# Kernel optimization log

Measured on AMD Instinct MI355X. Metric: run time of the kernel, lower is better.

The kernel has to match this reference:

```python
import jax, jax.numpy as jnp
import numpy as np

K_SAMPLES = 1024   # number of farthest-point samples (self.K)
K_NEIGH = 64       # neighbors per ball (self.k_classes)
RADIUS = 0.2       # ball-query radius
LAYERS = [64, 64, 128]
IN_CH = 3


def _fps_indices(pts, k):
    """Iterative farthest point sampling (pytorch3d-style, start at index 0).
    pts: (B, N, D) -> idx: (B, k) int32."""
    B, N, D = pts.shape
    big = jnp.asarray(1e10, pts.dtype)

    def step(carry, _):
        min_d, last = carry                                   # (B,N), (B,)
        lp = jnp.take_along_axis(pts, last[:, None, None], axis=1)  # (B,1,D)
        d = jnp.sum((pts - lp) ** 2, axis=-1)                 # (B,N)
        min_d = jnp.minimum(min_d, d)
        nxt = jnp.argmax(min_d, axis=-1).astype(jnp.int32)    # farthest so far
        return (min_d, nxt), nxt

    init = (jnp.full((B, N), big, pts.dtype), jnp.zeros((B,), jnp.int32))
    _, rest = jax.lax.scan(step, init, None, length=k - 1)    # (k-1, B)
    idx = jnp.concatenate([jnp.zeros((1, B), jnp.int32), rest], axis=0)
    return idx.T                                              # (B, k)


def _ball_query(queries, pts, k, radius):
    """For each query take the first k points of pts within radius (by index
    order, as in pytorch3d.ball_query); pad missing neighbors with zeros.
    queries: (B,K,D), pts: (B,N,D) -> grouped: (B,K,k,D)."""
    B, N, D = pts.shape
    q2 = jnp.sum(queries ** 2, axis=-1)                       # (B,K)
    p2 = jnp.sum(pts ** 2, axis=-1)                           # (B,N)
    d2 = q2[:, :, None] + p2[:, None, :] - 2.0 * jnp.einsum('bkd,bnd->bkn', queries, pts)
    valid = d2 < radius * radius                              # (B,K,N)
    arange_n = jnp.arange(N, dtype=jnp.int32)
    key = jnp.where(valid, arange_n, N)                       # invalid -> sentinel N
    neg_vals, nbr_idx = jax.lax.top_k(-key, k)                # k smallest keys
    taken_valid = (-neg_vals) < N                             # (B,K,k)
    grouped = jax.vmap(lambda p, i: p[i])(pts, nbr_idx)       # (B,K,k,D)
    grouped = jnp.where(taken_valid[..., None], grouped, jnp.zeros((), pts.dtype))
    return grouped


def setup_inputs() -> dict:
    key = jax.random.key(0)
    ks = jax.random.split(key, 7)
    points = jax.random.uniform(ks[0], (8, 4096, IN_CH), dtype=jnp.float32)
    dims = [IN_CH] + LAYERS
    inp = {'points': points}
    for li in range(len(LAYERS)):
        fan_in = dims[li]
        w = jax.random.normal(ks[1 + li], (dims[li], dims[li + 1]), dtype=jnp.float32) / np.sqrt(fan_in)
        b = jnp.zeros((dims[li + 1],), jnp.float32)
        inp[f'w{li}'] = w
        inp[f'b{li}'] = b
    return inp


def reference(points, w0, b0, w1, b1, w2, b2):
    # 1) farthest point sampling of K centroids
    fps_idx = _fps_indices(points, K_SAMPLES)                 # (B,K)
    selected = jax.vmap(lambda p, i: p[i])(points, fps_idx)   # (B,K,C)
    selected_xyz = selected[:, :, :3]
    # 2) ball query grouping around the centroids
    grouped = _ball_query(selected, points, K_NEIGH, RADIUS)  # (B,K,k,C)
    # 3) shared PointNet MLP (pointwise 1x1 conv == linear) + max-pool over neighbors
    h = grouped
    for w, b in ((w0, b0), (w1, b1), (w2, b2)):
        h = jax.nn.relu(jnp.einsum('bknc,cd->bknd', h, w) + b)
    feat = jnp.max(h, axis=2)                                 # (B,K,layers[-1])
    # 4) concat centroid xyz with pooled features
    return jnp.concatenate([selected_xyz, feat], axis=2)      # (B,K,3+128)
```

## Files before the change

### kernel.cpp

```cpp
#include <hip/hip_runtime.h>

#define BATCH 8
#define NPTS 4096
#define KSAMP 1024
#define KNEI 64
#define OUTC 131

typedef __attribute__((ext_vector_type(8))) short  bf16x8;
typedef __attribute__((ext_vector_type(4))) float  f32x4;

__device__ __forceinline__ unsigned short f2bf_rne(float f)
{
    unsigned u = __float_as_uint(f);
    return (unsigned short)((u + 0x7FFFu + ((u >> 16) & 1u)) >> 16);
}
__device__ __forceinline__ float bf2f(unsigned short h)
{
    return __uint_as_float(((unsigned)h) << 16);
}

__device__ __forceinline__ unsigned long long umax64(unsigned long long a,
                                                     unsigned long long b)
{
    return a > b ? a : b;
}

#define DPP_U64_STEP(v, CTRL)                                                  \
    {                                                                          \
        int _lo = __builtin_amdgcn_update_dpp(0, (int)(unsigned)(v), (CTRL),   \
                                              0xF, 0xF, true);                 \
        int _hi = __builtin_amdgcn_update_dpp(0, (int)((v) >> 32), (CTRL),     \
                                              0xF, 0xF, true);                 \
        unsigned long long _o =                                                \
            ((unsigned long long)(unsigned)_hi << 32) | (unsigned)_lo;         \
        (v) = umax64((v), _o);                                                 \
    }

__device__ __forceinline__ unsigned long long wave_umax64(unsigned long long v)
{
    DPP_U64_STEP(v, 0x111)
    DPP_U64_STEP(v, 0x112)
    DPP_U64_STEP(v, 0x114)
    DPP_U64_STEP(v, 0x118)
    DPP_U64_STEP(v, 0x142)
    DPP_U64_STEP(v, 0x143)
    return v;
}

#define DPP_F32MAX_STEP(v, CTRL)                                               \
    {                                                                          \
        int _s = __builtin_amdgcn_update_dpp(0, __float_as_int(v), (CTRL),     \
                                             0xF, 0xF, true);                  \
        (v) = fmaxf((v), __int_as_float(_s));                                  \
    }

__device__ __forceinline__ float wave_fmax_nonneg(float v)
{
    DPP_F32MAX_STEP(v, 0x111)
    DPP_F32MAX_STEP(v, 0x112)
    DPP_F32MAX_STEP(v, 0x114)
    DPP_F32MAX_STEP(v, 0x118)
    DPP_F32MAX_STEP(v, 0x142)
    DPP_F32MAX_STEP(v, 0x143)
    return v;
}

#define FPS_T 512
#define FPS_PPT 8
#define FPS_NW (FPS_T / 64)

__global__ __launch_bounds__(FPS_T) void fps_kernel(const float* __restrict__ pts,
                                                    float* __restrict__ out)
{
    const int b = blockIdx.x;
    const int t = threadIdx.x;
    const float* p = pts + (size_t)b * NPTS * 3;

    __shared__ float lx[NPTS], ly[NPTS], lz[NPTS];
    __shared__ unsigned long long cand[2][FPS_NW];

    float px[FPS_PPT], py[FPS_PPT], pz[FPS_PPT], md[FPS_PPT];
#pragma unroll
    for (int i = 0; i < FPS_PPT; ++i) {
        const int n = t * FPS_PPT + i;
        px[i] = p[n * 3 + 0];
        py[i] = p[n * 3 + 1];
        pz[i] = p[n * 3 + 2];
        lx[n] = px[i]; ly[n] = py[i]; lz[n] = pz[i];
        md[i] = 1e10f;
    }
    if (t == 0) {
        float* o = out + (size_t)b * KSAMP * OUTC;
        o[0] = p[0]; o[1] = p[1]; o[2] = p[2];
    }
    __syncthreads();

    const int wave = t >> 6;
    const int lane = t & 63;
    int cur = 0;

    for (int s = 1; s < KSAMP; ++s) {
        const float qx = lx[cur], qy = ly[cur], qz = lz[cur];

#pragma unroll
        for (int i = 0; i < FPS_PPT; ++i) {
            float dx = px[i] - qx, dy = py[i] - qy, dz = pz[i] - qz;
            float d = dx * dx + dy * dy + dz * dz;
            md[i] = fminf(md[i], d);
        }

        unsigned long long c[FPS_PPT];
#pragma unroll
        for (int i = 0; i < FPS_PPT; ++i)
            c[i] = ((unsigned long long)__float_as_uint(md[i]) << 32)
                 | (unsigned)(4095 - (t * FPS_PPT + i));
#pragma unroll
        for (int i = 0; i < 4; ++i) c[i] = umax64(c[i], c[i + 4]);
        c[0] = umax64(c[0], c[2]);
        c[1] = umax64(c[1], c[3]);
        unsigned long long best = umax64(c[0], c[1]);

        best = wave_umax64(best);
        const int par = s & 1;
        if (lane == 63) cand[par][wave] = best;
        __syncthreads();

        const unsigned long long g01 = umax64(cand[par][0], cand[par][1]);
        const unsigned long long g23 = umax64(cand[par][2], cand[par][3]);
        const unsigned long long g45 = umax64(cand[par][4], cand[par][5]);
        const unsigned long long g67 = umax64(cand[par][6], cand[par][7]);
        const unsigned long long g = umax64(umax64(g01, g23), umax64(g45, g67));
        cur = 4095 - (int)(g & 0xffffffffu);

        if (t == 0) {
            float* o = out + ((size_t)b * KSAMP + s) * OUTC;
            o[0] = lx[cur]; o[1] = ly[cur]; o[2] = lz[cur];
        }
    }
}

__global__ __launch_bounds__(256) void prep_kernel(const float* __restrict__ w1,
                                                   const float* __restrict__ w2,
                                                   unsigned short* __restrict__ ws)
{
    const int tid = blockIdx.x * 256 + threadIdx.x;
    if (tid >= 1536) return;
    const int fid  = tid >> 6;
    const int lane = tid & 63;
    const int lg = lane >> 4, lr = lane & 15;

    const float* W; int N, f; unsigned base_hi, base_lo;
    if (fid < 8) { W = w1; N = 64;  f = fid;     base_hi = 0;    base_lo = 4096; }
    else         { W = w2; N = 128; f = fid - 8; base_hi = 8192; base_lo = 16384; }
    const int nt = f >> 1, kc = f & 1;
    const int col = nt * 16 + lr;

    bf16x8 hi8, lo8;
#pragma unroll
    for (int i = 0; i < 8; ++i) {
        const int k = kc * 32 + lg * 8 + i;
        const float w = W[k * N + col];
        const unsigned short hs = f2bf_rne(w);
        hi8[i] = (short)hs;
        lo8[i] = (short)f2bf_rne(w - bf2f(hs));
    }
    ((bf16x8*)(ws + base_hi))[f * 64 + lane] = hi8;
    ((bf16x8*)(ws + base_lo))[f * 64 + lane] = lo8;
}

#define HPAD 72

__global__ __launch_bounds__(64) void bqmlp_mfma(
    const float* __restrict__ pts,
    const float* __restrict__ w0, const float* __restrict__ b0,
    const float* __restrict__ b1, const float* __restrict__ b2,
    const unsigned short* __restrict__ ws,
    float* __restrict__ out)
{
    const int q    = blockIdx.x;
    const int bb   = q >> 10;
    const int lane = threadIdx.x;
    const int lg   = lane >> 4, lr = lane & 15;
    const float* p = pts + (size_t)bb * NPTS * 3;
    float* orow    = out + (size_t)q * OUTC;

    __shared__ unsigned short hb_hi[64 * HPAD];
    __shared__ unsigned short hb_lo[64 * HPAD];
    __shared__ float snx[KNEI], sny[KNEI], snz[KNEI];

    const float qx = orow[0], qy = orow[1], qz = orow[2];
    const float RR = 0.04f;
    const float q2 = __fadd_rn(__fadd_rn(__fmul_rn(qx, qx), __fmul_rn(qy, qy)),
                               __fmul_rn(qz, qz));

    snx[lane] = 0.0f; sny[lane] = 0.0f; snz[lane] = 0.0f;
    __syncthreads();

    float cx = p[lane * 3 + 0];
    float cy = p[lane * 3 + 1];
    float cz = p[lane * 3 + 2];

    int total = 0;
#pragma unroll 4
    for (int c = 0; c < NPTS / 64; ++c) {
        const float x = cx, y = cy, z = cz;
        if (c + 1 < NPTS / 64) {
            const int n2 = (c + 1) * 64 + lane;
            cx = p[n2 * 3 + 0];
            cy = p[n2 * 3 + 1];
            cz = p[n2 * 3 + 2];
        }
        const float p2  = __fadd_rn(__fadd_rn(__fmul_rn(x, x), __fmul_rn(y, y)),
                                    __fmul_rn(z, z));
        const float dot = __fadd_rn(__fadd_rn(__fmul_rn(qx, x), __fmul_rn(qy, y)),
                                    __fmul_rn(qz, z));
        const float d2  = __fsub_rn(__fadd_rn(q2, p2), __fmul_rn(2.0f, dot));
        const bool valid = d2 < RR;
        const unsigned long long mask = __ballot(valid);
        const int pos = total + (int)__popcll(mask & ((1ull << lane) - 1ull));
        if (valid && pos < KNEI) { snx[pos] = x; sny[pos] = y; snz[pos] = z; }
        total += (int)__popcll(mask);
    }
    __syncthreads();

    const float x = snx[lane], y = sny[lane], z = snz[lane];

    float h0[64];
#pragma unroll
    for (int j = 0; j < 64; ++j) {
        float a = fmaf(x, w0[j], fmaf(y, w0[64 + j], fmaf(z, w0[128 + j], b0[j])));
        h0[j] = fmaxf(a, 0.0f);
    }

#pragma unroll
    for (int c = 0; c < 8; ++c) {
        bf16x8 hi8, lo8;
#pragma unroll
        for (int i = 0; i < 8; ++i) {
            const float v = h0[c * 8 + i];
            const unsigned short hs = f2bf_rne(v);
            hi8[i] = (short)hs;
            lo8[i] = (short)f2bf_rne(v - bf2f(hs));
        }
        *(bf16x8*)&hb_hi[lane * HPAD + c * 8] = hi8;
        *(bf16x8*)&hb_lo[lane * HPAD + c * 8] = lo8;
    }
    __syncthreads();

    const bf16x8* B1h = (const bf16x8*)ws;
    const bf16x8* B1l = B1h + 512;
    const bf16x8* B2h = B1h + 1024;
    const bf16x8* B2l = B1h + 2048;

    f32x4 acc2[4][4];
#pragma unroll
    for (int nt = 0; nt < 4; ++nt) {
        const float bv = b1[nt * 16 + lr];
#pragma unroll
        for (int mt = 0; mt < 4; ++mt)
            acc2[mt][nt] = (f32x4){bv, bv, bv, bv};
    }

#pragma unroll
    for (int mt = 0; mt < 4; ++mt) {
        bf16x8 ah[2], al[2];
#pragma unroll
        for (int kc = 0; kc < 2; ++kc) {
            ah[kc] = *(const bf16x8*)&hb_hi[(mt * 16 + lr) * HPAD + kc * 32 + lg * 8];
            al[kc] = *(const bf16x8*)&hb_lo[(mt * 16 + lr) * HPAD + kc * 32 + lg * 8];
        }
#pragma unroll
        for (int nt = 0; nt < 4; ++nt) {
#pragma unroll
            for (int kc = 0; kc < 2; ++kc) {
                const bf16x8 bh = B1h[(nt * 2 + kc) * 64 + lane];
                const bf16x8 bl = B1l[(nt * 2 + kc) * 64 + lane];
                acc2[mt][nt] = __builtin_amdgcn_mfma_f32_16x16x32_bf16(ah[kc], bh, acc2[mt][nt], 0, 0, 0);
                acc2[mt][nt] = __builtin_amdgcn_mfma_f32_16x16x32_bf16(ah[kc], bl, acc2[mt][nt], 0, 0, 0);
                acc2[mt][nt] = __builtin_amdgcn_mfma_f32_16x16x32_bf16(al[kc], bh, acc2[mt][nt], 0, 0, 0);
            }
        }
    }

    __syncthreads();
#pragma unroll
    for (int mt = 0; mt < 4; ++mt) {
#pragma unroll
        for (int nt = 0; nt < 4; ++nt) {
#pragma unroll
            for (int r = 0; r < 4; ++r) {
                const float v = fmaxf(acc2[mt][nt][r], 0.0f);
                const int row = mt * 16 + lg * 4 + r;
                const int col = nt * 16 + lr;
                const unsigned short hs = f2bf_rne(v);
                hb_hi[row * HPAD + col] = hs;
                hb_lo[row * HPAD + col] = f2bf_rne(v - bf2f(hs));
            }
        }
    }
    __syncthreads();

#pragma unroll
    for (int h = 0; h < 2; ++h) {
        f32x4 acc3[4][4];
#pragma unroll
        for (int nt4 = 0; nt4 < 4; ++nt4) {
            const float bv = b2[(h * 4 + nt4) * 16 + lr];
#pragma unroll
            for (int mt = 0; mt < 4; ++mt)
                acc3[mt][nt4] = (f32x4){bv, bv, bv, bv};
        }

#pragma unroll
        for (int mt = 0; mt < 4; ++mt) {
            bf16x8 ah[2], al[2];
#pragma unroll
            for (int kc = 0; kc < 2; ++kc) {
                ah[kc] = *(const bf16x8*)&hb_hi[(mt * 16 + lr) * HPAD + kc * 32 + lg * 8];
                al[kc] = *(const bf16x8*)&hb_lo[(mt * 16 + lr) * HPAD + kc * 32 + lg * 8];
            }
#pragma unroll
            for (int nt4 = 0; nt4 < 4; ++nt4) {
                const int f = (h * 4 + nt4) * 2;
#pragma unroll
                for (int kc = 0; kc < 2; ++kc) {
                    const bf16x8 bh = B2h[(f + kc) * 64 + lane];
                    const bf16x8 bl = B2l[(f + kc) * 64 + lane];
                    acc3[mt][nt4] = __builtin_amdgcn_mfma_f32_16x16x32_bf16(ah[kc], bh, acc3[mt][nt4], 0, 0, 0);
                    acc3[mt][nt4] = __builtin_amdgcn_mfma_f32_16x16x32_bf16(ah[kc], bl, acc3[mt][nt4], 0, 0, 0);
                    acc3[mt][nt4] = __builtin_amdgcn_mfma_f32_16x16x32_bf16(al[kc], bh, acc3[mt][nt4], 0, 0, 0);
                }
            }
        }

#pragma unroll
        for (int nt4 = 0; nt4 < 4; ++nt4) {
            float m = 0.0f;
#pragma unroll
            for (int mt = 0; mt < 4; ++mt)
#pragma unroll
                for (int r = 0; r < 4; ++r)
                    m = fmaxf(m, acc3[mt][nt4][r]);
            m = fmaxf(m, __shfl_xor(m, 16));
            m = fmaxf(m, __shfl_xor(m, 32));
            if (lane < 16) orow[3 + (h * 4 + nt4) * 16 + lane] = m;
        }
    }
}

__global__ __launch_bounds__(64) void bqmlp_fp32(
    const float* __restrict__ pts,
    const float* __restrict__ w0, const float* __restrict__ b0,
    const float* __restrict__ w1, const float* __restrict__ b1,
    const float* __restrict__ w2, const float* __restrict__ b2,
    float* __restrict__ out)
{
    const int q    = blockIdx.x;
    const int bb   = q >> 10;
    const int lane = threadIdx.x;
    const float* p = pts + (size_t)bb * NPTS * 3;
    float* orow    = out + (size_t)q * OUTC;

    const float qx = orow[0], qy = orow[1], qz = orow[2];
    const float RR = 0.04f;
    const float q2 = __fadd_rn(__fadd_rn(__fmul_rn(qx, qx), __fmul_rn(qy, qy)),
                               __fmul_rn(qz, qz));

    __shared__ float nx[KNEI], ny[KNEI], nz[KNEI];
    nx[lane] = 0.0f; ny[lane] = 0.0f; nz[lane] = 0.0f;
    __syncthreads();

    int total = 0;
    for (int c = 0; c < NPTS / 64 && total < KNEI; ++c) {
        const int n = c * 64 + lane;
        const float x = p[n * 3 + 0];
        const float y = p[n * 3 + 1];
        const float z = p[n * 3 + 2];
        const float p2  = __fadd_rn(__fadd_rn(__fmul_rn(x, x), __fmul_rn(y, y)),
                                    __fmul_rn(z, z));
        const float dot = __fadd_rn(__fadd_rn(__fmul_rn(qx, x), __fmul_rn(qy, y)),
                                    __fmul_rn(qz, z));
        const float d2  = __fsub_rn(__fadd_rn(q2, p2), __fmul_rn(2.0f, dot));
        const bool valid = d2 < RR;
        const unsigned long long mask = __ballot(valid);
        const int pos = total + (int)__popcll(mask & ((1ull << lane) - 1ull));
        if (valid && pos < KNEI) { nx[pos] = x; ny[pos] = y; nz[pos] = z; }
        total += (int)__popcll(mask);
    }
    __syncthreads();

    const float x = nx[lane], y = ny[lane], z = nz[lane];

    float h0[64];
#pragma unroll
    for (int j = 0; j < 64; ++j) {
        float a = fmaf(x, w0[j], fmaf(y, w0[64 + j], fmaf(z, w0[128 + j], b0[j])));
        h0[j] = fmaxf(a, 0.0f);
    }

    float h1[64];
#pragma unroll
    for (int jb = 0; jb < 4; ++jb) {
        float acc[16];
#pragma unroll
        for (int i = 0; i < 16; ++i) acc[i] = b1[jb * 16 + i];
#pragma unroll
        for (int k = 0; k < 64; ++k) {
#pragma unroll
            for (int i = 0; i < 16; ++i)
                acc[i] = fmaf(h0[k], w1[k * 64 + jb * 16 + i], acc[i]);
        }
#pragma unroll
        for (int i = 0; i < 16; ++i) h1[jb * 16 + i] = fmaxf(acc[i], 0.0f);
    }

#pragma unroll
    for (int jb = 0; jb < 8; ++jb) {
        float acc[16];
#pragma unroll
        for (int i = 0; i < 16; ++i) acc[i] = b2[jb * 16 + i];
#pragma unroll
        for (int k = 0; k < 64; ++k) {
#pragma unroll
            for (int i = 0; i < 16; ++i)
                acc[i] = fmaf(h1[k], w2[k * 128 + jb * 16 + i], acc[i]);
        }
#pragma unroll
        for (int i = 0; i < 16; ++i) {
            float v = fmaxf(acc[i], 0.0f);
            acc[i] = wave_fmax_nonneg(v);
        }
        if (lane == 63) {
#pragma unroll
            for (int i = 0; i < 16; ++i) orow[3 + jb * 16 + i] = acc[i];
        }
    }
}

extern "C" void kernel_launch(void* const* d_in, const int* in_sizes, int n_in,
                              void* d_out, int out_size, void* d_ws, size_t ws_size,
                              hipStream_t stream)
{
    (void)in_sizes; (void)n_in; (void)out_size;
    const float* pts = (const float*)d_in[0];
    const float* w0  = (const float*)d_in[1];
    const float* b0  = (const float*)d_in[2];
    const float* w1  = (const float*)d_in[3];
    const float* b1  = (const float*)d_in[4];
    const float* w2  = (const float*)d_in[5];
    const float* b2  = (const float*)d_in[6];
    float* out = (float*)d_out;

    hipLaunchKernelGGL(fps_kernel, dim3(BATCH), dim3(FPS_T), 0, stream, pts, out);

    if (ws_size >= 49152) {
        unsigned short* wsp = (unsigned short*)d_ws;
        hipLaunchKernelGGL(prep_kernel, dim3(6), dim3(256), 0, stream, w1, w2, wsp);
        hipLaunchKernelGGL(bqmlp_mfma, dim3(BATCH * KSAMP), dim3(64), 0, stream,
                           pts, w0, b0, b1, b2, wsp, out);
    } else {
        hipLaunchKernelGGL(bqmlp_fp32, dim3(BATCH * KSAMP), dim3(64), 0, stream,
                           pts, w0, b0, w1, b1, w2, b2, out);
    }
}
```

Before: 802.9 us.

## Fuse FPS and ball-query MLP into one cooperative kernel with progress flags

Replaces the separate FPS and per-query MLP launches with one cooperative persistent kernel. Eight blocks run FPS and publish progress counters every 32 samples, while the other waves poll those counters and process queries whose centroids are ready. The long serial FPS phase can then overlap with the MLP work. FPS also moves from 512 threads to 256 threads with 16 points per thread, and per-wave syncthreads become waitcnt fences. The cost is spin-waiting, reliance on the cooperative launch succeeding, and FPS blocks sharing CUs with MLP waves, which may slow the critical FPS path.

```diff
diff --git a/kernel.cpp b/kernel.cpp
--- a/kernel.cpp
+++ b/kernel.cpp
@@ -1,10 +1,14 @@
 #include <hip/hip_runtime.h>
+#include <hip/hip_cooperative_groups.h>
+
+namespace cg = cooperative_groups;
 
 #define BATCH 8
 #define NPTS 4096
 #define KSAMP 1024
 #define KNEI 64
 #define OUTC 131
+#define HPAD 72
 
 typedef __attribute__((ext_vector_type(8))) short  bf16x8;
 typedef __attribute__((ext_vector_type(4))) float  f32x4;
@@ -17,6 +21,11 @@
 __device__ __forceinline__ float bf2f(unsigned short h)
 {
     return __uint_as_float(((unsigned)h) << 16);
+}
+
+__device__ __forceinline__ void lds_fence()
+{
+    asm volatile("s_waitcnt lgkmcnt(0)" ::: "memory");
 }
 
 __device__ __forceinline__ unsigned long long umax64(unsigned long long a,
@@ -65,20 +74,15 @@
     return v;
 }
 
-#define FPS_T 512
-#define FPS_PPT 8
-#define FPS_NW (FPS_T / 64)
-
-__global__ __launch_bounds__(FPS_T) void fps_kernel(const float* __restrict__ pts,
-                                                    float* __restrict__ out)
-{
-    const int b = blockIdx.x;
-    const int t = threadIdx.x;
-    const float* p = pts + (size_t)b * NPTS * 3;
-
-    __shared__ float lx[NPTS], ly[NPTS], lz[NPTS];
-    __shared__ unsigned long long cand[2][FPS_NW];
-
+#define FPS_T 256
+#define FPS_PPT 16
+
+__device__ __forceinline__ void fps_body(const float* __restrict__ p,
+                                         float* __restrict__ outB,
+                                         float* lx, float* ly, float* lz,
+                                         unsigned long long* cand,
+                                         unsigned* prog, int b, int t)
+{
     float px[FPS_PPT], py[FPS_PPT], pz[FPS_PPT], md[FPS_PPT];
 #pragma unroll
     for (int i = 0; i < FPS_PPT; ++i) {
@@ -89,10 +93,7 @@
         lx[n] = px[i]; ly[n] = py[i]; lz[n] = pz[i];
         md[i] = 1e10f;
     }
-    if (t == 0) {
-        float* o = out + (size_t)b * KSAMP * OUTC;
-        o[0] = p[0]; o[1] = p[1]; o[2] = p[2];
-    }
+    if (t == 0) { outB[0] = p[0]; outB[1] = p[1]; outB[2] = p[2]; }
     __syncthreads();
 
     const int wave = t >> 6;
@@ -115,6 +116,8 @@
             c[i] = ((unsigned long long)__float_as_uint(md[i]) << 32)
                  | (unsigned)(4095 - (t * FPS_PPT + i));
 #pragma unroll
+        for (int i = 0; i < 8; ++i) c[i] = umax64(c[i], c[i + 8]);
+#pragma unroll
         for (int i = 0; i < 4; ++i) c[i] = umax64(c[i], c[i + 4]);
         c[0] = umax64(c[0], c[2]);
         c[1] = umax64(c[1], c[3]);
@@ -122,19 +125,19 @@
 
         best = wave_umax64(best);
         const int par = s & 1;
-        if (lane == 63) cand[par][wave] = best;
+        if (lane == 63) cand[par * 4 + wave] = best;
         __syncthreads();
 
-        const unsigned long long g01 = umax64(cand[par][0], cand[par][1]);
-        const unsigned long long g23 = umax64(cand[par][2], cand[par][3]);
-        const unsigned long long g45 = umax64(cand[par][4], cand[par][5]);
-        const unsigned long long g67 = umax64(cand[par][6], cand[par][7]);
-        const unsigned long long g = umax64(umax64(g01, g23), umax64(g45, g67));
+        unsigned long long g = umax64(umax64(cand[par * 4 + 0], cand[par * 4 + 1]),
+                                      umax64(cand[par * 4 + 2], cand[par * 4 + 3]));
         cur = 4095 - (int)(g & 0xffffffffu);
 
         if (t == 0) {
-            float* o = out + ((size_t)b * KSAMP + s) * OUTC;
+            float* o = outB + (size_t)s * OUTC;
             o[0] = lx[cur]; o[1] = ly[cur]; o[2] = lz[cur];
+            if (prog && (s & 31) == 31)
+                __hip_atomic_store(&prog[b], (unsigned)(s + 1),
+                                   __ATOMIC_RELEASE, __HIP_MEMORY_SCOPE_AGENT);
         }
     }
 }
@@ -168,33 +171,28 @@
     ((bf16x8*)(ws + base_lo))[f * 64 + lane] = lo8;
 }
 
-#define HPAD 72
-
-__global__ __launch_bounds__(64) void bqmlp_mfma(
+__device__ __forceinline__ void mlp_wave(
+    int q, int lane,
     const float* __restrict__ pts,
     const float* __restrict__ w0, const float* __restrict__ b0,
     const float* __restrict__ b1, const float* __restrict__ b2,
-    const unsigned short* __restrict__ ws,
-    float* __restrict__ out)
-{
-    const int q    = blockIdx.x;
-    const int bb   = q >> 10;
-    const int lane = threadIdx.x;
-    const int lg   = lane >> 4, lr = lane & 15;
+    const unsigned short* __restrict__ wfrag,
+    float* __restrict__ out,
+    unsigned short* hb_hi, unsigned short* hb_lo,
+    float* snx, float* sny, float* snz)
+{
+    const int bb = q >> 10;
+    const int lg = lane >> 4, lr = lane & 15;
     const float* p = pts + (size_t)bb * NPTS * 3;
     float* orow    = out + (size_t)q * OUTC;
-
-    __shared__ unsigned short hb_hi[64 * HPAD];
-    __shared__ unsigned short hb_lo[64 * HPAD];
-    __shared__ float snx[KNEI], sny[KNEI], snz[KNEI];
 
     const float qx = orow[0], qy = orow[1], qz = orow[2];
     const float RR = 0.04f;
     const float q2 = __fadd_rn(__fadd_rn(__fmul_rn(qx, qx), __fmul_rn(qy, qy)),
                                __fmul_rn(qz, qz));
 
+    lds_fence();
     snx[lane] = 0.0f; sny[lane] = 0.0f; snz[lane] = 0.0f;
-    __syncthreads();
 
     float cx = p[lane * 3 + 0];
     float cy = p[lane * 3 + 1];
@@ -221,7 +219,7 @@
         if (valid && pos < KNEI) { snx[pos] = x; sny[pos] = y; snz[pos] = z; }
         total += (int)__popcll(mask);
     }
-    __syncthreads();
+    lds_fence();
 
     const float x = snx[lane], y = sny[lane], z = snz[lane];
 
@@ -245,9 +243,9 @@
         *(bf16x8*)&hb_hi[lane * HPAD + c * 8] = hi8;
         *(bf16x8*)&hb_lo[lane * HPAD + c * 8] = lo8;
     }
-    __syncthreads();
-
-    const bf16x8* B1h = (const bf16x8*)ws;
+    lds_fence();
+
+    const bf16x8* B1h = (const bf16x8*)wfrag;
     const bf16x8* B1l = B1h + 512;
     const bf16x8* B2h = B1h + 1024;
     const bf16x8* B2l = B1h + 2048;
@@ -282,7 +280,7 @@
         }
     }
 
-    __syncthreads();
+    lds_fence();
 #pragma unroll
     for (int mt = 0; mt < 4; ++mt) {
 #pragma unroll
@@ -298,7 +296,7 @@
             }
         }
     }
-    __syncthreads();
+    lds_fence();
 
 #pragma unroll
     for (int h = 0; h < 2; ++h) {
@@ -346,6 +344,78 @@
             if (lane < 16) orow[3 + (h * 4 + nt4) * 16 + lane] = m;
         }
     }
+}
+
+__global__ __launch_bounds__(256) void fused_kernel(
+    const float* __restrict__ pts,
+    const float* __restrict__ w0, const float* __restrict__ b0,
+    const float* __restrict__ b1, const float* __restrict__ b2,
+    const unsigned short* __restrict__ wfrag,
+    unsigned* __restrict__ prog,
+    float* __restrict__ out)
+{
+    __shared__ union {
+        struct {
+            float lx[NPTS], ly[NPTS], lz[NPTS];
+            unsigned long long cand[8];
+        } f;
+        struct {
+            unsigned short hb_hi[64 * HPAD];
+            unsigned short hb_lo[64 * HPAD];
+            float snx[KNEI], sny[KNEI], snz[KNEI];
+        } m[4];
+    } smem;
+
+    const int t = threadIdx.x;
+
+    if (blockIdx.x == 0 && t < BATCH)
+        __hip_atomic_store(&prog[t], 0u, __ATOMIC_RELAXED, __HIP_MEMORY_SCOPE_AGENT);
+    cg::this_grid().sync();
+
+    if (blockIdx.x < BATCH) {
+        const int b = blockIdx.x;
+        fps_body(pts + (size_t)b * NPTS * 3, out + (size_t)b * KSAMP * OUTC,
+                 smem.f.lx, smem.f.ly, smem.f.lz, smem.f.cand, prog, b, t);
+        __syncthreads();
+    }
+
+    const int wv = t >> 6, lane = t & 63;
+    const int wave_id = blockIdx.x * 4 + wv;
+    for (int q = wave_id; q < BATCH * KSAMP; q += 1024) {
+        const int bb = q >> 10;
+        const unsigned need = (unsigned)((q & 1023) + 1);
+        while (__hip_atomic_load(&prog[bb], __ATOMIC_RELAXED,
+                                 __HIP_MEMORY_SCOPE_AGENT) < need)
+            __builtin_amdgcn_s_sleep(64);
+        (void)__hip_atomic_load(&prog[bb], __ATOMIC_ACQUIRE,
+                                __HIP_MEMORY_SCOPE_AGENT);
+        mlp_wave(q, lane, pts, w0, b0, b1, b2, wfrag, out,
+                 smem.m[wv].hb_hi, smem.m[wv].hb_lo,
+                 smem.m[wv].snx, smem.m[wv].sny, smem.m[wv].snz);
+    }
+}
+
+__global__ __launch_bounds__(FPS_T) void fps_kernel(const float* __restrict__ pts,
+                                                    float* __restrict__ out)
+{
+    __shared__ float lx[NPTS], ly[NPTS], lz[NPTS];
+    __shared__ unsigned long long cand[8];
+    fps_body(pts + (size_t)blockIdx.x * NPTS * 3,
+             out + (size_t)blockIdx.x * KSAMP * OUTC,
+             lx, ly, lz, cand, nullptr, blockIdx.x, threadIdx.x);
+}
+
+__global__ __launch_bounds__(64) void bqmlp_mfma(
+    const float* __restrict__ pts,
+    const float* __restrict__ w0, const float* __restrict__ b0,
+    const float* __restrict__ b1, const float* __restrict__ b2,
+    const unsigned short* __restrict__ wfrag,
+    float* __restrict__ out)
+{
+    __shared__ unsigned short hb_hi[64 * HPAD], hb_lo[64 * HPAD];
+    __shared__ float snx[KNEI], sny[KNEI], snz[KNEI];
+    mlp_wave(blockIdx.x, threadIdx.x, pts, w0, b0, b1, b2, wfrag, out,
+             hb_hi, hb_lo, snx, sny, snz);
 }
 
 __global__ __launch_bounds__(64) void bqmlp_fp32(
@@ -451,15 +521,26 @@
     const float* b2  = (const float*)d_in[6];
     float* out = (float*)d_out;
 
+    if (ws_size >= 49152 + 256) {
+        unsigned* prog = (unsigned*)d_ws;
+        unsigned short* wfrag = (unsigned short*)d_ws + 128;
+        hipLaunchKernelGGL(prep_kernel, dim3(6), dim3(256), 0, stream, w1, w2, wfrag);
+
+        void* args[8] = { (void*)&pts, (void*)&w0, (void*)&b0, (void*)&b1,
+                          (void*)&b2, (void*)&wfrag, (void*)&prog, (void*)&out };
+        hipError_t e = hipLaunchCooperativeKernel((const void*)fused_kernel,
+                                                  dim3(256), dim3(256),
+                                                  args, 0, stream);
+        if (e == hipSuccess) return;
+        (void)hipGetLastError();
+
+        hipLaunchKernelGGL(fps_kernel, dim3(BATCH), dim3(FPS_T), 0, stream, pts, out);
+        hipLaunchKernelGGL(bqmlp_mfma, dim3(BATCH * KSAMP), dim3(64), 0, stream,
+                           pts, w0, b0, b1, b2, wfrag, out);
+        return;
+    }
+
     hipLaunchKernelGGL(fps_kernel, dim3(BATCH), dim3(FPS_T), 0, stream, pts, out);
-
-    if (ws_size >= 49152) {
-        unsigned short* wsp = (unsigned short*)d_ws;
-        hipLaunchKernelGGL(prep_kernel, dim3(6), dim3(256), 0, stream, w1, w2, wsp);
-        hipLaunchKernelGGL(bqmlp_mfma, dim3(BATCH * KSAMP), dim3(64), 0, stream,
-                           pts, w0, b0, b1, b2, wsp, out);
-    } else {
-        hipLaunchKernelGGL(bqmlp_fp32, dim3(BATCH * KSAMP), dim3(64), 0, stream,
-                           pts, w0, b0, w1, b1, w2, b2, out);
-    }
-}
+    hipLaunchKernelGGL(bqmlp_fp32, dim3(BATCH * KSAMP), dim3(64), 0, stream,
+                       pts, w0, b0, w1, b1, w2, b2, out);
+}
```

Result: slower. 893.7 us (+11.3%).

## Shrink FPS block, batch centroid stores via LDS ring, drop single-wave barriers

Applied to the files above, without the earlier changes.

The FPS kernel moves from 512 to 256 threads with 16 points per thread, so the cross-wave reduction covers 4 waves instead of 8. Selected centroid coordinates now go into a 64-entry LDS ring and are flushed to global memory every 32 steps by 96 threads, replacing a per-iteration single-thread global store. In the single-wave ball-query/MLP kernel, __syncthreads is replaced with an lgkmcnt wait, which relies on one wave per block. The ring flush reads entries written by thread 0 without a barrier in between, which depends on the next iteration's barrier and may be fragile.

```diff
diff --git a/kernel.cpp b/kernel.cpp
--- a/kernel.cpp
+++ b/kernel.cpp
@@ -5,6 +5,7 @@
 #define KSAMP 1024
 #define KNEI 64
 #define OUTC 131
+#define HPAD 72
 
 typedef __attribute__((ext_vector_type(8))) short  bf16x8;
 typedef __attribute__((ext_vector_type(4))) float  f32x4;
@@ -17,6 +18,11 @@
 __device__ __forceinline__ float bf2f(unsigned short h)
 {
     return __uint_as_float(((unsigned)h) << 16);
+}
+
+__device__ __forceinline__ void lds_fence()
+{
+    asm volatile("s_waitcnt lgkmcnt(0)" ::: "memory");
 }
 
 __device__ __forceinline__ unsigned long long umax64(unsigned long long a,
@@ -47,27 +53,8 @@
     return v;
 }
 
-#define DPP_F32MAX_STEP(v, CTRL)                                               \
-    {                                                                          \
-        int _s = __builtin_amdgcn_update_dpp(0, __float_as_int(v), (CTRL),     \
-                                             0xF, 0xF, true);                  \
-        (v) = fmaxf((v), __int_as_float(_s));                                  \
-    }
-
-__device__ __forceinline__ float wave_fmax_nonneg(float v)
-{
-    DPP_F32MAX_STEP(v, 0x111)
-    DPP_F32MAX_STEP(v, 0x112)
-    DPP_F32MAX_STEP(v, 0x114)
-    DPP_F32MAX_STEP(v, 0x118)
-    DPP_F32MAX_STEP(v, 0x142)
-    DPP_F32MAX_STEP(v, 0x143)
-    return v;
-}
-
-#define FPS_T 512
-#define FPS_PPT 8
-#define FPS_NW (FPS_T / 64)
+#define FPS_T 256
+#define FPS_PPT 16
 
 __global__ __launch_bounds__(FPS_T) void fps_kernel(const float* __restrict__ pts,
                                                     float* __restrict__ out)
@@ -75,9 +62,11 @@
     const int b = blockIdx.x;
     const int t = threadIdx.x;
     const float* p = pts + (size_t)b * NPTS * 3;
+    float* outB    = out + (size_t)b * KSAMP * OUTC;
 
     __shared__ float lx[NPTS], ly[NPTS], lz[NPTS];
-    __shared__ unsigned long long cand[2][FPS_NW];
+    __shared__ unsigned long long cand[8];
+    __shared__ float ring[64 * 3];
 
     float px[FPS_PPT], py[FPS_PPT], pz[FPS_PPT], md[FPS_PPT];
 #pragma unroll
@@ -89,10 +78,7 @@
         lx[n] = px[i]; ly[n] = py[i]; lz[n] = pz[i];
         md[i] = 1e10f;
     }
-    if (t == 0) {
-        float* o = out + (size_t)b * KSAMP * OUTC;
-        o[0] = p[0]; o[1] = p[1]; o[2] = p[2];
-    }
+    if (t == 0) { outB[0] = p[0]; outB[1] = p[1]; outB[2] = p[2]; }
     __syncthreads();
 
     const int wave = t >> 6;
@@ -115,6 +101,8 @@
             c[i] = ((unsigned long long)__float_as_uint(md[i]) << 32)
                  | (unsigned)(4095 - (t * FPS_PPT + i));
 #pragma unroll
+        for (int i = 0; i < 8; ++i) c[i] = umax64(c[i], c[i + 8]);
+#pragma unroll
         for (int i = 0; i < 4; ++i) c[i] = umax64(c[i], c[i + 4]);
         c[0] = umax64(c[0], c[2]);
         c[1] = umax64(c[1], c[3]);
@@ -122,20 +110,33 @@
 
         best = wave_umax64(best);
         const int par = s & 1;
-        if (lane == 63) cand[par][wave] = best;
+        if (lane == 63) cand[par * 4 + wave] = best;
         __syncthreads();
 
-        const unsigned long long g01 = umax64(cand[par][0], cand[par][1]);
-        const unsigned long long g23 = umax64(cand[par][2], cand[par][3]);
-        const unsigned long long g45 = umax64(cand[par][4], cand[par][5]);
-        const unsigned long long g67 = umax64(cand[par][6], cand[par][7]);
-        const unsigned long long g = umax64(umax64(g01, g23), umax64(g45, g67));
+        unsigned long long g = umax64(umax64(cand[par * 4 + 0], cand[par * 4 + 1]),
+                                      umax64(cand[par * 4 + 2], cand[par * 4 + 3]));
         cur = 4095 - (int)(g & 0xffffffffu);
 
         if (t == 0) {
-            float* o = out + ((size_t)b * KSAMP + s) * OUTC;
-            o[0] = lx[cur]; o[1] = ly[cur]; o[2] = lz[cur];
-        }
+            float* r = ring + (s & 63) * 3;
+            r[0] = lx[cur]; r[1] = ly[cur]; r[2] = lz[cur];
+        }
+
+        if ((s & 31) == 0) {
+            if (t < 96) {
+                const int row  = s - 32 + t / 3;
+                const int comp = t % 3;
+                if (row >= 1)
+                    outB[(size_t)row * OUTC + comp] = ring[(row & 63) * 3 + comp];
+            }
+        }
+    }
+
+    __syncthreads();
+    if (t < 96) {
+        const int row  = 992 + t / 3;
+        const int comp = t % 3;
+        outB[(size_t)row * OUTC + comp] = ring[(row & 63) * 3 + comp];
     }
 }
 
@@ -168,13 +169,11 @@
     ((bf16x8*)(ws + base_lo))[f * 64 + lane] = lo8;
 }
 
-#define HPAD 72
-
 __global__ __launch_bounds__(64) void bqmlp_mfma(
     const float* __restrict__ pts,
     const float* __restrict__ w0, const float* __restrict__ b0,
     const float* __restrict__ b1, const float* __restrict__ b2,
-    const unsigned short* __restrict__ ws,
+    const unsigned short* __restrict__ wfrag,
     float* __restrict__ out)
 {
     const int q    = blockIdx.x;
@@ -194,7 +193,7 @@
                                __fmul_rn(qz, qz));
 
     snx[lane] = 0.0f; sny[lane] = 0.0f; snz[lane] = 0.0f;
-    __syncthreads();
+    lds_fence();
 
     float cx = p[lane * 3 + 0];
     float cy = p[lane * 3 + 1];
@@ -221,7 +220,7 @@
         if (valid && pos < KNEI) { snx[pos] = x; sny[pos] = y; snz[pos] = z; }
         total += (int)__popcll(mask);
     }
-    __syncthreads();
+    lds_fence();
 
     const float x = snx[lane], y = sny[lane], z = snz[lane];
 
@@ -245,9 +244,9 @@
         *(bf16x8*)&hb_hi[lane * HPAD + c * 8] = hi8;
         *(bf16x8*)&hb_lo[lane * HPAD + c * 8] = lo8;
     }
-    __syncthreads();
-
-    const bf16x8* B1h = (const bf16x8*)ws;
+    lds_fence();
+
+    const bf16x8* B1h = (const bf16x8*)wfrag;
     const bf16x8* B1l = B1h + 512;
     const bf16x8* B2h = B1h + 1024;
     const bf16x8* B2l = B1h + 2048;
@@ -282,7 +281,7 @@
         }
     }
 
-    __syncthreads();
+    lds_fence();
 #pragma unroll
     for (int mt = 0; mt < 4; ++mt) {
 #pragma unroll
@@ -298,7 +297,7 @@
             }
         }
     }
-    __syncthreads();
+    lds_fence();
 
 #pragma unroll
     for (int h = 0; h < 2; ++h) {
@@ -346,6 +345,24 @@
             if (lane < 16) orow[3 + (h * 4 + nt4) * 16 + lane] = m;
         }
     }
+}
+
+#define DPP_F32MAX_STEP(v, CTRL)                                               \
+    {                                                                          \
+        int _s = __builtin_amdgcn_update_dpp(0, __float_as_int(v), (CTRL),     \
+                                             0xF, 0xF, true);                  \
+        (v) = fmaxf((v), __int_as_float(_s));                                  \
+    }
+
+__device__ __forceinline__ float wave_fmax_nonneg(float v)
+{
+    DPP_F32MAX_STEP(v, 0x111)
+    DPP_F32MAX_STEP(v, 0x112)
+    DPP_F32MAX_STEP(v, 0x114)
+    DPP_F32MAX_STEP(v, 0x118)
+    DPP_F32MAX_STEP(v, 0x142)
+    DPP_F32MAX_STEP(v, 0x143)
+    return v;
 }
 
 __global__ __launch_bounds__(64) void bqmlp_fp32(
@@ -454,10 +471,10 @@
     hipLaunchKernelGGL(fps_kernel, dim3(BATCH), dim3(FPS_T), 0, stream, pts, out);
 
     if (ws_size >= 49152) {
-        unsigned short* wsp = (unsigned short*)d_ws;
-        hipLaunchKernelGGL(prep_kernel, dim3(6), dim3(256), 0, stream, w1, w2, wsp);
+        unsigned short* wfrag = (unsigned short*)d_ws;
+        hipLaunchKernelGGL(prep_kernel, dim3(6), dim3(256), 0, stream, w1, w2, wfrag);
         hipLaunchKernelGGL(bqmlp_mfma, dim3(BATCH * KSAMP), dim3(64), 0, stream,
-                           pts, w0, b0, b1, b2, wsp, out);
+                           pts, w0, b0, b1, b2, wfrag, out);
     } else {
         hipLaunchKernelGGL(bqmlp_fp32, dim3(BATCH * KSAMP), dim3(64), 0, stream,
                            pts, w0, b0, w1, b1, w2, b2, out);
```

Result: slower. 820.1 us (+2.1%).
